# Kernel optimization log

Hardware: AMD Instinct MI355X
Metric: run time of the kernel (lower is better)

Reference implementation:

```python
import jax, jax.numpy as jnp
import numpy as np

S, B, SC = 2048, 1024, 256 * 16  # shops, bundles, styles*colors


def setup_inputs() -> dict:
    key = jax.random.key(0)
    k1, k2, k3, k4 = jax.random.split(key, 4)
    return {
        "proba": jax.random.normal(k1, (S * B,), dtype=jnp.float32),
        "cur_inven": jax.random.uniform(k2, (S, SC), dtype=jnp.float32),
        "bun_sc": jax.random.uniform(k3, (B, SC), dtype=jnp.float32),
        "avail_bundle": jax.random.uniform(k4, (B,), dtype=jnp.float32),
        "alloc_bundle": jnp.zeros((B,), dtype=jnp.float32),
    }


def reference(proba, cur_inven, bun_sc, avail_bundle, alloc_bundle):
    # proba[i] with i = shop*B + bundle  ->  [S, B]
    p = proba.reshape(S, B)
    # constraint_multiplier: 0.01 if over-availability (p>0) or over-negative-alloc (p<0)
    over_avail = (avail_bundle[None, :] - p < 0.0) & (p > 0.0)
    over_alloc = (alloc_bundle[None, :] + p < 0.0) & (p < 0.0)
    cm = jnp.where(over_avail | over_alloc, jnp.float32(0.01), jnp.float32(1.0))
    # next_inven[s, sc] = cur[s, sc] + sum_b bun_sc[b, sc] * p[s, b] * cm[s, b]
    next_inven = cur_inven + jnp.einsum('sb,bc->sc', p * cm, bun_sc)
    return next_inven.reshape(1, -1)
```

## Files before the change

### kernel.cpp

```cpp
#include <hip/hip_runtime.h>

#define S_DIM  2048
#define B_DIM  1024
#define SC_DIM 4096

#define BM 128
#define BN 128
#define BK 64

typedef __bf16 bf16x8 __attribute__((ext_vector_type(8)));
typedef float  f32x4  __attribute__((ext_vector_type(4)));
typedef unsigned short u16x4 __attribute__((ext_vector_type(4)));
typedef unsigned short u16x8 __attribute__((ext_vector_type(8)));

__device__ __forceinline__ unsigned short f2bf(float f) {
    unsigned int u = __builtin_bit_cast(unsigned int, f);
    return (unsigned short)((u + 0x7FFFu + ((u >> 16) & 1u)) >> 16);
}

__device__ __forceinline__ void gld_lds16(const void* g, void* l) {
    __builtin_amdgcn_global_load_lds(
        (const __attribute__((address_space(1))) unsigned int*)g,
        (__attribute__((address_space(3))) unsigned int*)l, 16, 0, 0);
}

__global__ __launch_bounds__(256)
void prepack_ab(const float* __restrict__ proba,
                const float* __restrict__ avail,
                const float* __restrict__ alloc,
                const float* __restrict__ bsc,
                unsigned short* __restrict__ wsA,
                unsigned short* __restrict__ wsB)
{
    __shared__ float lds[64][129];
    const int t = threadIdx.x;

    if (blockIdx.x < 1024) {
        int c = blockIdx.x * 256 + t;
        int n = c >> 7;
        int G = c & 127;
        int k = G * 8;

        f32x4 p0 = *(const f32x4*)&proba[(size_t)n * B_DIM + k];
        f32x4 p1 = *(const f32x4*)&proba[(size_t)n * B_DIM + k + 4];
        f32x4 av0 = *(const f32x4*)&avail[k];
        f32x4 av1 = *(const f32x4*)&avail[k + 4];
        f32x4 al0 = *(const f32x4*)&alloc[k];
        f32x4 al1 = *(const f32x4*)&alloc[k + 4];

        u16x8 w;
        #pragma unroll
        for (int i = 0; i < 4; ++i) {
            float pv = p0[i];
            bool oa = (av0[i] - pv < 0.f) && (pv > 0.f);
            bool ob = (al0[i] + pv < 0.f) && (pv < 0.f);
            w[i] = f2bf(pv * ((oa || ob) ? 0.01f : 1.0f));
        }
        #pragma unroll
        for (int i = 0; i < 4; ++i) {
            float pv = p1[i];
            bool oa = (av1[i] - pv < 0.f) && (pv > 0.f);
            bool ob = (al1[i] + pv < 0.f) && (pv < 0.f);
            w[4 + i] = f2bf(pv * ((oa || ob) ? 0.01f : 1.0f));
        }
        int Gs = (G & ~7) | ((G & 7) ^ (n & 7));
        *(u16x8*)&wsA[(size_t)n * B_DIM + Gs * 8] = w;
    } else {
        int b2 = blockIdx.x - 1024;
        const int bn0 = (b2 & 31) * 128;
        const int k0  = (b2 >> 5) * 64;

        #pragma unroll
        for (int p = 0; p < 8; ++p) {
            int kl = (t >> 5) + p * 8;
            int cl = (t & 31) * 4;
            f32x4 v = *(const f32x4*)&bsc[(size_t)(k0 + kl) * SC_DIM + bn0 + cl];
            lds[kl][cl]     = v[0];
            lds[kl][cl + 1] = v[1];
            lds[kl][cl + 2] = v[2];
            lds[kl][cl + 3] = v[3];
        }
        __syncthreads();

        #pragma unroll
        for (int p = 0; p < 4; ++p) {
            int g = t & 7;
            int n = (t >> 3) + p * 32;
            u16x8 w;
            #pragma unroll
            for (int i = 0; i < 8; ++i)
                w[i] = f2bf(lds[g * 8 + i][n]);
            int gs = g ^ (n & 7);
            *(u16x8*)&wsB[(size_t)(bn0 + n) * B_DIM + k0 + gs * 8] = w;
        }
    }
}

__global__ __launch_bounds__(256, 2)
void gemm_pk(const unsigned short* __restrict__ wsA,
             const unsigned short* __restrict__ wsB,
             const float* __restrict__ cur,
             float* __restrict__ out)
{
    __shared__ __align__(16) unsigned short sA[BM * BK];
    __shared__ __align__(16) unsigned short sB[BN * BK];

    const int tid  = threadIdx.x;
    const int lane = tid & 63;
    const int wid  = tid >> 6;
    const int wm   = wid >> 1;
    const int wn   = wid & 1;
    const int l16  = lane & 15;
    const int lg   = lane >> 4;

    const int bid    = blockIdx.x;
    const int x      = bid & 7;
    const int l      = bid >> 3;
    const int n_tile = x * 4 + (l & 3);
    const int m_tile = l >> 2;
    const int bm0    = m_tile * BM;
    const int bn0    = n_tile * BN;

    const int crow = tid >> 3;
    const int cg   = tid & 7;

    f32x4 acc[4][4];
    #pragma unroll
    for (int i = 0; i < 4; ++i)
        #pragma unroll
        for (int j = 0; j < 4; ++j)
            acc[i][j] = {0.f, 0.f, 0.f, 0.f};

    auto stage = [&](int k0) {
        #pragma unroll
        for (int is = 0; is < 4; ++is)
            gld_lds16(wsA + (size_t)(bm0 + is * 32 + crow) * B_DIM + k0 + cg * 8,
                      &sA[(is * 256 + tid) * 8]);
        #pragma unroll
        for (int is = 0; is < 4; ++is)
            gld_lds16(wsB + (size_t)(bn0 + is * 32 + crow) * B_DIM + k0 + cg * 8,
                      &sB[(is * 256 + tid) * 8]);
    };

    stage(0);

    float cpre[2][4];

    #pragma unroll
    for (int t = 0; t < 16; ++t) {
        __syncthreads();

        if (t >= 8) {
            #pragma unroll
            for (int u = 0; u < 2; ++u) {
                const int s  = 2 * (t - 8) + u;
                const int mf = s >> 2, nf = s & 3;
                #pragma unroll
                for (int j = 0; j < 4; ++j)
                    acc[mf][nf][j] += cpre[u][j];
            }
        }

        bf16x8 afr[2][4], bfr[2][4];
        #pragma unroll
        for (int kk = 0; kk < 2; ++kk) {
            #pragma unroll
            for (int mf = 0; mf < 4; ++mf) {
                int r = wm * 64 + mf * 16 + l16;
                afr[kk][mf] = *(const bf16x8*)&sA[r * BK + (((kk * 4 + lg) ^ (r & 7)) * 8)];
            }
            #pragma unroll
            for (int nf = 0; nf < 4; ++nf) {
                int r = wn * 64 + nf * 16 + l16;
                bfr[kk][nf] = *(const bf16x8*)&sB[r * BK + (((kk * 4 + lg) ^ (r & 7)) * 8)];
            }
        }
        __syncthreads();

        if (t < 15)
            stage((t + 1) * BK);

        if (t >= 7 && t < 15) {
            #pragma unroll
            for (int u = 0; u < 2; ++u) {
                const int s   = 2 * (t - 7) + u;
                const int mf  = s >> 2, nf = s & 3;
                const int row = bm0 + wm * 64 + mf * 16 + lg * 4;
                const int col = bn0 + wn * 64 + nf * 16 + l16;
                #pragma unroll
                for (int j = 0; j < 4; ++j)
                    cpre[u][j] = cur[(size_t)(row + j) * SC_DIM + col];
            }
        }
        __builtin_amdgcn_sched_barrier(0);

        #pragma unroll
        for (int kk = 0; kk < 2; ++kk)
            #pragma unroll
            for (int mf = 0; mf < 4; ++mf)
                #pragma unroll
                for (int nf = 0; nf < 4; ++nf)
                    acc[mf][nf] = __builtin_amdgcn_mfma_f32_16x16x32_bf16(
                        afr[kk][mf], bfr[kk][nf], acc[kk ? mf : mf][nf], 0, 0, 0);
    }

    #pragma unroll
    for (int mf = 0; mf < 4; ++mf)
        #pragma unroll
        for (int j = 0; j < 4; ++j)
            #pragma unroll
            for (int nf = 0; nf < 4; ++nf) {
                int row = bm0 + wm * 64 + mf * 16 + lg * 4 + j;
                int col = bn0 + wn * 64 + nf * 16 + l16;
                out[(size_t)row * SC_DIM + col] = acc[mf][nf][j];
            }
}

#define FBM 128
#define FBN 128
#define LDK 72
__global__ __launch_bounds__(256, 2)
void opt_gemm_fused(const float* __restrict__ proba,
                    const float* __restrict__ cur,
                    const float* __restrict__ bsc,
                    const float* __restrict__ avail,
                    const float* __restrict__ alloc,
                    float* __restrict__ out)
{
    __shared__ __align__(16) unsigned short sA[FBM * LDK];
    __shared__ __align__(16) unsigned short sB[FBN * LDK];
    const int tid = threadIdx.x;
    const int lane = tid & 63;
    const int wid = tid >> 6;
    const int wm = wid >> 1, wn = wid & 1;
    const int bm0 = blockIdx.y * FBM, bn0 = blockIdx.x * FBN;
    const int af4 = tid & 15, ar0 = tid >> 4;
    const int bnn = tid & 127, bkh = tid >> 7;
    const int l16 = lane & 15, lg = lane >> 4;

    f32x4 acc[4][4];
    #pragma unroll
    for (int i = 0; i < 4; ++i)
        #pragma unroll
        for (int j = 0; j < 4; ++j) acc[i][j] = {0.f, 0.f, 0.f, 0.f};

    for (int k0 = 0; k0 < B_DIM; k0 += BK) {
        f32x4 av = *(const f32x4*)&avail[k0 + af4 * 4];
        f32x4 al = *(const f32x4*)&alloc[k0 + af4 * 4];
        #pragma unroll
        for (int pass = 0; pass < 8; ++pass) {
            int r = ar0 + pass * 16;
            f32x4 p = *(const f32x4*)&proba[(size_t)(bm0 + r) * B_DIM + k0 + af4 * 4];
            u16x4 w;
            #pragma unroll
            for (int i = 0; i < 4; ++i) {
                float pv = p[i];
                bool oa = (av[i] - pv < 0.f) && (pv > 0.f);
                bool ob = (al[i] + pv < 0.f) && (pv < 0.f);
                w[i] = f2bf(pv * ((oa || ob) ? 0.01f : 1.0f));
            }
            *(u16x4*)&sA[r * LDK + af4 * 4] = w;
        }
        #pragma unroll
        for (int g = 0; g < 4; ++g) {
            u16x8 w;
            #pragma unroll
            for (int i = 0; i < 8; ++i) {
                int kk = bkh * 32 + g * 8 + i;
                w[i] = f2bf(bsc[(size_t)(k0 + kk) * SC_DIM + bn0 + bnn]);
            }
            *(u16x8*)&sB[bnn * LDK + bkh * 32 + g * 8] = w;
        }
        __syncthreads();
        #pragma unroll
        for (int kk = 0; kk < 2; ++kk) {
            bf16x8 afr[4], bfr[4];
            #pragma unroll
            for (int mf = 0; mf < 4; ++mf)
                afr[mf] = *(const bf16x8*)&sA[(wm * 64 + mf * 16 + l16) * LDK + kk * 32 + lg * 8];
            #pragma unroll
            for (int nf = 0; nf < 4; ++nf)
                bfr[nf] = *(const bf16x8*)&sB[(wn * 64 + nf * 16 + l16) * LDK + kk * 32 + lg * 8];
            #pragma unroll
            for (int mf = 0; mf < 4; ++mf)
                #pragma unroll
                for (int nf = 0; nf < 4; ++nf)
                    acc[mf][nf] = __builtin_amdgcn_mfma_f32_16x16x32_bf16(
                        afr[mf], bfr[nf], acc[mf][nf], 0, 0, 0);
        }
        __syncthreads();
    }
    #pragma unroll
    for (int mf = 0; mf < 4; ++mf)
        #pragma unroll
        for (int j = 0; j < 4; ++j) {
            int row = bm0 + wm * 64 + mf * 16 + lg * 4 + j;
            #pragma unroll
            for (int nf = 0; nf < 4; ++nf) {
                int col = bn0 + wn * 64 + nf * 16 + l16;
                size_t idx = (size_t)row * SC_DIM + col;
                out[idx] = cur[idx] + acc[mf][nf][j];
            }
        }
}

extern "C" void kernel_launch(void* const* d_in, const int* in_sizes, int n_in,
                              void* d_out, int out_size, void* d_ws, size_t ws_size,
                              hipStream_t stream) {
    const float* proba = (const float*)d_in[0];
    const float* cur   = (const float*)d_in[1];
    const float* bsc   = (const float*)d_in[2];
    const float* avail = (const float*)d_in[3];
    const float* alloc = (const float*)d_in[4];
    float* out = (float*)d_out;

    const size_t wsA_bytes = (size_t)S_DIM * B_DIM * 2;
    const size_t wsB_bytes = (size_t)SC_DIM * B_DIM * 2;

    if (ws_size >= wsA_bytes + wsB_bytes) {
        unsigned short* wsA = (unsigned short*)d_ws;
        unsigned short* wsB = (unsigned short*)((char*)d_ws + wsA_bytes);

        prepack_ab<<<dim3(1024 + 512), 256, 0, stream>>>(proba, avail, alloc, bsc, wsA, wsB);
        gemm_pk<<<dim3((S_DIM / BM) * (SC_DIM / BN)), 256, 0, stream>>>(wsA, wsB, cur, out);
    } else {
        opt_gemm_fused<<<dim3(SC_DIM / FBN, S_DIM / FBM), 256, 0, stream>>>(
            proba, cur, bsc, avail, alloc, out);
    }
}
```

Before: 35.69 us.

## Double-buffer LDS tiles with two-stage prefetch and explicit vmcnt waits

Allocates two LDS buffers for the A and B tiles and prefetches two K-steps ahead, so global-to-LDS loads for step t+2 are issued while step t is being computed. The full __syncthreads is replaced by manual s_waitcnt vmcnt counts plus s_barrier, with the count set according to how many cur loads are in flight. This is meant to hide global load latency behind the MFMA work. In exchange it doubles LDS use, which may lower occupancy, and the correctness of the hand-tuned vmcnt values depends on the exact order in which loads are issued.

```diff
diff --git a/kernel.cpp b/kernel.cpp
--- a/kernel.cpp
+++ b/kernel.cpp
@@ -23,6 +23,10 @@
         (const __attribute__((address_space(1))) unsigned int*)g,
         (__attribute__((address_space(3))) unsigned int*)l, 16, 0, 0);
 }
+
+#define VMW8()  asm volatile("s_waitcnt vmcnt(8)"  ::: "memory")
+#define VMW16() asm volatile("s_waitcnt vmcnt(16)" ::: "memory")
+#define LGKM0() asm volatile("s_waitcnt lgkmcnt(0)" ::: "memory")
 
 __global__ __launch_bounds__(256)
 void prepack_ab(const float* __restrict__ proba,
@@ -102,8 +106,8 @@
              const float* __restrict__ cur,
              float* __restrict__ out)
 {
-    __shared__ __align__(16) unsigned short sA[BM * BK];
-    __shared__ __align__(16) unsigned short sB[BN * BK];
+    __shared__ __align__(16) unsigned short sA[2][BM * BK];
+    __shared__ __align__(16) unsigned short sB[2][BN * BK];
 
     const int tid  = threadIdx.x;
     const int lane = tid & 63;
@@ -131,24 +135,28 @@
         for (int j = 0; j < 4; ++j)
             acc[i][j] = {0.f, 0.f, 0.f, 0.f};
 
-    auto stage = [&](int k0) {
+    auto stage = [&](int k0, int buf) {
         #pragma unroll
         for (int is = 0; is < 4; ++is)
             gld_lds16(wsA + (size_t)(bm0 + is * 32 + crow) * B_DIM + k0 + cg * 8,
-                      &sA[(is * 256 + tid) * 8]);
+                      &sA[buf][(is * 256 + tid) * 8]);
         #pragma unroll
         for (int is = 0; is < 4; ++is)
             gld_lds16(wsB + (size_t)(bn0 + is * 32 + crow) * B_DIM + k0 + cg * 8,
-                      &sB[(is * 256 + tid) * 8]);
+                      &sB[buf][(is * 256 + tid) * 8]);
     };
 
-    stage(0);
+    stage(0, 0);
+    stage(BK, 1);
 
     float cpre[2][4];
 
     #pragma unroll
     for (int t = 0; t < 16; ++t) {
-        __syncthreads();
+        const int buf = t & 1;
+
+        if (t >= 8 && t <= 14) { VMW16(); } else { VMW8(); }
+        __builtin_amdgcn_s_barrier();
 
         if (t >= 8) {
             #pragma unroll
@@ -167,20 +175,19 @@
             #pragma unroll
             for (int mf = 0; mf < 4; ++mf) {
                 int r = wm * 64 + mf * 16 + l16;
-                afr[kk][mf] = *(const bf16x8*)&sA[r * BK + (((kk * 4 + lg) ^ (r & 7)) * 8)];
+                afr[kk][mf] = *(const bf16x8*)&sA[buf][r * BK + (((kk * 4 + lg) ^ (r & 7)) * 8)];
             }
             #pragma unroll
             for (int nf = 0; nf < 4; ++nf) {
                 int r = wn * 64 + nf * 16 + l16;
-                bfr[kk][nf] = *(const bf16x8*)&sB[r * BK + (((kk * 4 + lg) ^ (r & 7)) * 8)];
-            }
-        }
-        __syncthreads();
-
-        if (t < 15)
-            stage((t + 1) * BK);
-
-        if (t >= 7 && t < 15) {
+                bfr[kk][nf] = *(const bf16x8*)&sB[buf][r * BK + (((kk * 4 + lg) ^ (r & 7)) * 8)];
+            }
+        }
+        LGKM0();
+        __builtin_amdgcn_sched_barrier(0);
+        __builtin_amdgcn_s_barrier();
+
+        if (t >= 7 && t <= 14) {
             #pragma unroll
             for (int u = 0; u < 2; ++u) {
                 const int s   = 2 * (t - 7) + u;
@@ -192,6 +199,8 @@
                     cpre[u][j] = cur[(size_t)(row + j) * SC_DIM + col];
             }
         }
+        if (t <= 13)
+            stage((t + 2) * BK, buf);
         __builtin_amdgcn_sched_barrier(0);
 
         #pragma unroll
@@ -201,7 +210,7 @@
                 #pragma unroll
                 for (int nf = 0; nf < 4; ++nf)
                     acc[mf][nf] = __builtin_amdgcn_mfma_f32_16x16x32_bf16(
-                        afr[kk][mf], bfr[kk][nf], acc[kk ? mf : mf][nf], 0, 0, 0);
+                        afr[kk][mf], bfr[kk][nf], acc[mf][nf], 0, 0, 0);
     }
 
     #pragma unroll
```

Result: no change. 35.75 us (+0.2%).

## Prepack operands in MFMA fragment order and load directly into registers

Applied to the files above, without the earlier changes.

The prepack kernel now writes A and B in per-lane MFMA fragment order, so each wave's operand fragment is one contiguous 1 KB chunk. The GEMM kernel drops LDS staging and its barriers, loads fragments straight from global memory into registers, and double-buffers them across k-steps with ping-pong register sets. This removes LDS traffic and block-level synchronisation. In exchange, A and B tiles shared between waves are fetched once per wave instead of once per block, which leans on L2, and register pressure rises.

```diff
diff --git a/kernel.cpp b/kernel.cpp
--- a/kernel.cpp
+++ b/kernel.cpp
@@ -4,24 +4,13 @@
 #define B_DIM  1024
 #define SC_DIM 4096
 
-#define BM 128
-#define BN 128
-#define BK 64
-
 typedef __bf16 bf16x8 __attribute__((ext_vector_type(8)));
 typedef float  f32x4  __attribute__((ext_vector_type(4)));
-typedef unsigned short u16x4 __attribute__((ext_vector_type(4)));
 typedef unsigned short u16x8 __attribute__((ext_vector_type(8)));
 
 __device__ __forceinline__ unsigned short f2bf(float f) {
     unsigned int u = __builtin_bit_cast(unsigned int, f);
     return (unsigned short)((u + 0x7FFFu + ((u >> 16) & 1u)) >> 16);
-}
-
-__device__ __forceinline__ void gld_lds16(const void* g, void* l) {
-    __builtin_amdgcn_global_load_lds(
-        (const __attribute__((address_space(1))) unsigned int*)g,
-        (__attribute__((address_space(3))) unsigned int*)l, 16, 0, 0);
 }
 
 __global__ __launch_bounds__(256)
@@ -37,12 +26,15 @@
 
     if (blockIdx.x < 1024) {
         int c = blockIdx.x * 256 + t;
-        int n = c >> 7;
-        int G = c & 127;
-        int k = G * 8;
-
-        f32x4 p0 = *(const f32x4*)&proba[(size_t)n * B_DIM + k];
-        f32x4 p1 = *(const f32x4*)&proba[(size_t)n * B_DIM + k + 4];
+        int lane = c & 63;
+        int slot = c >> 6;
+        int mg = slot >> 5;
+        int kb = slot & 31;
+        int row = mg * 16 + (lane & 15);
+        int k   = kb * 32 + (lane >> 4) * 8;
+
+        f32x4 p0 = *(const f32x4*)&proba[(size_t)row * B_DIM + k];
+        f32x4 p1 = *(const f32x4*)&proba[(size_t)row * B_DIM + k + 4];
         f32x4 av0 = *(const f32x4*)&avail[k];
         f32x4 av1 = *(const f32x4*)&avail[k + 4];
         f32x4 al0 = *(const f32x4*)&alloc[k];
@@ -63,8 +55,7 @@
             bool ob = (al1[i] + pv < 0.f) && (pv < 0.f);
             w[4 + i] = f2bf(pv * ((oa || ob) ? 0.01f : 1.0f));
         }
-        int Gs = (G & ~7) | ((G & 7) ^ (n & 7));
-        *(u16x8*)&wsA[(size_t)n * B_DIM + Gs * 8] = w;
+        *(u16x8*)&wsA[(size_t)c * 8] = w;
     } else {
         int b2 = blockIdx.x - 1024;
         const int bn0 = (b2 & 31) * 128;
@@ -82,29 +73,31 @@
         }
         __syncthreads();
 
-        #pragma unroll
-        for (int p = 0; p < 4; ++p) {
-            int g = t & 7;
-            int n = (t >> 3) + p * 32;
+        const int g    = t >> 6;
+        const int lane = t & 63;
+        #pragma unroll
+        for (int q = 0; q < 4; ++q) {
+            int f   = g * 4 + q;
+            int ngl = f >> 1;
+            int kbl = f & 1;
+            int nl  = ngl * 16 + (lane & 15);
+            int kl  = kbl * 32 + (lane >> 4) * 8;
             u16x8 w;
             #pragma unroll
             for (int i = 0; i < 8; ++i)
-                w[i] = f2bf(lds[g * 8 + i][n]);
-            int gs = g ^ (n & 7);
-            *(u16x8*)&wsB[(size_t)(bn0 + n) * B_DIM + k0 + gs * 8] = w;
+                w[i] = f2bf(lds[kl + i][nl]);
+            size_t slot = ((size_t)(bn0 / 16 + ngl) * 32 + (k0 / 32 + kbl)) * 64 + lane;
+            *(u16x8*)&wsB[slot * 8] = w;
         }
     }
 }
 
 __global__ __launch_bounds__(256, 2)
-void gemm_pk(const unsigned short* __restrict__ wsA,
+void gemm_rf(const unsigned short* __restrict__ wsA,
              const unsigned short* __restrict__ wsB,
              const float* __restrict__ cur,
              float* __restrict__ out)
 {
-    __shared__ __align__(16) unsigned short sA[BM * BK];
-    __shared__ __align__(16) unsigned short sB[BN * BK];
-
     const int tid  = threadIdx.x;
     const int lane = tid & 63;
     const int wid  = tid >> 6;
@@ -118,11 +111,11 @@
     const int l      = bid >> 3;
     const int n_tile = x * 4 + (l & 3);
     const int m_tile = l >> 2;
-    const int bm0    = m_tile * BM;
-    const int bn0    = n_tile * BN;
-
-    const int crow = tid >> 3;
-    const int cg   = tid & 7;
+    const int row0   = m_tile * 128 + wm * 64;
+    const int col0   = n_tile * 128 + wn * 64;
+
+    const unsigned short* aBase = wsA + ((size_t)(row0 >> 4) * 32 * 64 + lane) * 8;
+    const unsigned short* bBase = wsB + ((size_t)(col0 >> 4) * 32 * 64 + lane) * 8;
 
     f32x4 acc[4][4];
     #pragma unroll
@@ -131,25 +124,24 @@
         for (int j = 0; j < 4; ++j)
             acc[i][j] = {0.f, 0.f, 0.f, 0.f};
 
-    auto stage = [&](int k0) {
-        #pragma unroll
-        for (int is = 0; is < 4; ++is)
-            gld_lds16(wsA + (size_t)(bm0 + is * 32 + crow) * B_DIM + k0 + cg * 8,
-                      &sA[(is * 256 + tid) * 8]);
-        #pragma unroll
-        for (int is = 0; is < 4; ++is)
-            gld_lds16(wsB + (size_t)(bn0 + is * 32 + crow) * B_DIM + k0 + cg * 8,
-                      &sB[(is * 256 + tid) * 8]);
+    auto loadset = [&](int t, bf16x8 (&a)[2][4], bf16x8 (&b)[2][4]) {
+        #pragma unroll
+        for (int kk = 0; kk < 2; ++kk) {
+            #pragma unroll
+            for (int f = 0; f < 4; ++f) {
+                a[kk][f] = *(const bf16x8*)(aBase + (size_t)(f * 32 + 2 * t + kk) * 512);
+                b[kk][f] = *(const bf16x8*)(bBase + (size_t)(f * 32 + 2 * t + kk) * 512);
+            }
+        }
     };
 
-    stage(0);
-
+    bf16x8 aP[2][4], bP[2][4], aQ[2][4], bQ[2][4];
     float cpre[2][4];
 
-    #pragma unroll
-    for (int t = 0; t < 16; ++t) {
-        __syncthreads();
-
+    loadset(0, aP, bP);
+
+    auto body = [&](int t, bf16x8 (&aC)[2][4], bf16x8 (&bC)[2][4],
+                    bf16x8 (&aN)[2][4], bf16x8 (&bN)[2][4]) {
         if (t >= 8) {
             #pragma unroll
             for (int u = 0; u < 2; ++u) {
@@ -161,38 +153,21 @@
             }
         }
 
-        bf16x8 afr[2][4], bfr[2][4];
-        #pragma unroll
-        for (int kk = 0; kk < 2; ++kk) {
-            #pragma unroll
-            for (int mf = 0; mf < 4; ++mf) {
-                int r = wm * 64 + mf * 16 + l16;
-                afr[kk][mf] = *(const bf16x8*)&sA[r * BK + (((kk * 4 + lg) ^ (r & 7)) * 8)];
-            }
-            #pragma unroll
-            for (int nf = 0; nf < 4; ++nf) {
-                int r = wn * 64 + nf * 16 + l16;
-                bfr[kk][nf] = *(const bf16x8*)&sB[r * BK + (((kk * 4 + lg) ^ (r & 7)) * 8)];
-            }
-        }
-        __syncthreads();
-
         if (t < 15)
-            stage((t + 1) * BK);
+            loadset(t + 1, aN, bN);
 
         if (t >= 7 && t < 15) {
             #pragma unroll
             for (int u = 0; u < 2; ++u) {
                 const int s   = 2 * (t - 7) + u;
                 const int mf  = s >> 2, nf = s & 3;
-                const int row = bm0 + wm * 64 + mf * 16 + lg * 4;
-                const int col = bn0 + wn * 64 + nf * 16 + l16;
+                const int row = row0 + mf * 16 + lg * 4;
+                const int col = col0 + nf * 16 + l16;
                 #pragma unroll
                 for (int j = 0; j < 4; ++j)
                     cpre[u][j] = cur[(size_t)(row + j) * SC_DIM + col];
             }
         }
-        __builtin_amdgcn_sched_barrier(0);
 
         #pragma unroll
         for (int kk = 0; kk < 2; ++kk)
@@ -201,7 +176,13 @@
                 #pragma unroll
                 for (int nf = 0; nf < 4; ++nf)
                     acc[mf][nf] = __builtin_amdgcn_mfma_f32_16x16x32_bf16(
-                        afr[kk][mf], bfr[kk][nf], acc[kk ? mf : mf][nf], 0, 0, 0);
+                        aC[kk][mf], bC[kk][nf], acc[mf][nf], 0, 0, 0);
+    };
+
+    #pragma unroll
+    for (int tt = 0; tt < 8; ++tt) {
+        body(2 * tt,     aP, bP, aQ, bQ);
+        body(2 * tt + 1, aQ, bQ, aP, bP);
     }
 
     #pragma unroll
@@ -210,8 +191,8 @@
         for (int j = 0; j < 4; ++j)
             #pragma unroll
             for (int nf = 0; nf < 4; ++nf) {
-                int row = bm0 + wm * 64 + mf * 16 + lg * 4 + j;
-                int col = bn0 + wn * 64 + nf * 16 + l16;
+                int row = row0 + mf * 16 + lg * 4 + j;
+                int col = col0 + nf * 16 + l16;
                 out[(size_t)row * SC_DIM + col] = acc[mf][nf][j];
             }
 }
@@ -244,14 +225,14 @@
         #pragma unroll
         for (int j = 0; j < 4; ++j) acc[i][j] = {0.f, 0.f, 0.f, 0.f};
 
-    for (int k0 = 0; k0 < B_DIM; k0 += BK) {
+    for (int k0 = 0; k0 < B_DIM; k0 += 64) {
         f32x4 av = *(const f32x4*)&avail[k0 + af4 * 4];
         f32x4 al = *(const f32x4*)&alloc[k0 + af4 * 4];
         #pragma unroll
         for (int pass = 0; pass < 8; ++pass) {
             int r = ar0 + pass * 16;
             f32x4 p = *(const f32x4*)&proba[(size_t)(bm0 + r) * B_DIM + k0 + af4 * 4];
-            u16x4 w;
+            unsigned short w[4];
             #pragma unroll
             for (int i = 0; i < 4; ++i) {
                 float pv = p[i];
@@ -259,7 +240,10 @@
                 bool ob = (al[i] + pv < 0.f) && (pv < 0.f);
                 w[i] = f2bf(pv * ((oa || ob) ? 0.01f : 1.0f));
             }
-            *(u16x4*)&sA[r * LDK + af4 * 4] = w;
+            sA[r * LDK + af4 * 4 + 0] = w[0];
+            sA[r * LDK + af4 * 4 + 1] = w[1];
+            sA[r * LDK + af4 * 4 + 2] = w[2];
+            sA[r * LDK + af4 * 4 + 3] = w[3];
         }
         #pragma unroll
         for (int g = 0; g < 4; ++g) {
@@ -322,7 +306,7 @@
         unsigned short* wsB = (unsigned short*)((char*)d_ws + wsA_bytes);
 
         prepack_ab<<<dim3(1024 + 512), 256, 0, stream>>>(proba, avail, alloc, bsc, wsA, wsB);
-        gemm_pk<<<dim3((S_DIM / BM) * (SC_DIM / BN)), 256, 0, stream>>>(wsA, wsB, cur, out);
+        gemm_rf<<<dim3(512), 256, 0, stream>>>(wsA, wsB, cur, out);
     } else {
         opt_gemm_fused<<<dim3(SC_DIM / FBN, S_DIM / FBM), 256, 0, stream>>>(
             proba, cur, bsc, avail, alloc, out);
```

New measurement: 57.09 us. 1.6x slower.
